# Kernel optimization log

Measured on AMD Instinct MI355X. Metric: run time of the kernel, lower is better.

## Reference

```python
import jax, jax.numpy as jnp
import numpy as np
from functools import partial

# Regular Tanner graph: (dv=3, dc=6)-regular LDPC-style code
NUM_CHKS = 512
NUM_VARS = 1024
DC = 6           # check degree
DV = 3           # variable degree
D = 16           # msg_dim
HIDDEN_MULT = 4
T = 5
BATCH = 256
E = NUM_CHKS * DC  # = NUM_VARS * DV = 3072 edges


def setup_inputs() -> dict:
    key = jax.random.key(0)
    ks = jax.random.split(key, 12)

    syndromes = jax.random.randint(ks[0], (BATCH, NUM_CHKS), 0, 2, dtype=jnp.int32)

    # Graph: edge e (check-major) belongs to check e//DC, slot e%DC.
    # perm lists edge ids in var-major order: perm[v*DV + s] = edge id.
    rng = np.random.default_rng(0)
    perm = jnp.asarray(rng.permutation(E), dtype=jnp.int32)

    prior_llr = jax.random.normal(ks[1], (NUM_VARS,), dtype=jnp.float32)

    in_c = DC * D + 1          # 97
    hid_c = HIDDEN_MULT * in_c # 388
    out_c = DC * D             # 96
    in_v = DV * D + 1          # 49
    hid_v = HIDDEN_MULT * in_v # 196
    out_v = DV * D + 1         # 49

    def lin(k, fan_in, fan_out):
        lim = 1.0 / np.sqrt(fan_in)
        kw, kb = jax.random.split(k)
        W = jax.random.uniform(kw, (fan_in, fan_out), jnp.float32, -lim, lim)
        b = jax.random.uniform(kb, (fan_out,), jnp.float32, -lim, lim)
        return W, b

    cW1, cb1 = lin(ks[2], in_c, hid_c)
    cW2, cb2 = lin(ks[3], hid_c, out_c)
    vW1, vb1 = lin(ks[4], in_v, hid_v)
    vW2, vb2 = lin(ks[5], hid_v, out_v)

    return {
        "syndromes": syndromes, "num_iters": T, "prior_llr": prior_llr,
        "perm": perm, "cW1": cW1, "cb1": cb1, "cW2": cW2, "cb2": cb2,
        "vW1": vW1, "vb1": vb1, "vW2": vW2, "vb2": vb2,
    }


def _mlp(x, W1, b1, W2, b2):
    h = jax.nn.gelu(x @ W1 + b1, approximate=False)  # torch nn.GELU default = exact
    return h @ W2 + b2


def reference(syndromes, num_iters, prior_llr, perm, cW1, cb1, cW2, cb2, vW1, vb1, vW2, vb2):
    B = syndromes.shape[0]
    sgn = (1 - 2 * syndromes).astype(jnp.float32)          # (B, C) syndrome signs
    inv_perm = jnp.argsort(perm)                            # edge -> var-major slot
    var_of_edge = inv_perm // DV                            # (E,)

    # Init var->check messages: first component = prior LLR of the edge's variable
    Mc0 = jnp.zeros((B, E, D), jnp.float32).at[:, :, 0].set(
        jnp.broadcast_to(prior_llr[var_of_edge][None, :], (B, E)))

    prior_col = jnp.broadcast_to(prior_llr[None, :, None], (B, NUM_VARS, 1))

    def step(Mc, _):
        # --- check node update (all checks have degree DC; grouped GEMM) ---
        xc = Mc.reshape(B, NUM_CHKS, DC * D)
        xc = jnp.concatenate([xc, sgn[:, :, None]], axis=-1)        # (B,C,DC*D+1)
        yc = _mlp(xc, cW1, cb1, cW2, cb2) * sgn[:, :, None]         # (B,C,DC*D)
        Mv = yc.reshape(B, E, D)                                     # check->var msgs (edge order)
        # --- variable node update (all vars have degree DV) ---
        xv = Mv[:, perm].reshape(B, NUM_VARS, DV * D)                # gather var-major
        xv = jnp.concatenate([xv, prior_col], axis=-1)               # (B,V,DV*D+1)
        yv = _mlp(xv, vW1, vb1, vW2, vb2)                            # (B,V,DV*D+1)
        llr = yv[:, :, -1]                                           # (B,V)
        Mc_new = yv[:, :, : DV * D].reshape(B, E, D)[:, inv_perm]    # scatter to edge order
        return Mc_new, llr

    _, llrs = jax.lax.scan(step, Mc0, None, length=num_iters)
    return llrs  # (T, B, NUM_VARS)
```

## Files before the change

### kernel.cpp

```cpp
#include <hip/hip_runtime.h>
#include <cstdint>
#include <cstddef>

typedef _Float16 half8 __attribute__((ext_vector_type(8)));
typedef _Float16 half4 __attribute__((ext_vector_type(4)));
typedef float floatx4 __attribute__((ext_vector_type(4)));

#define BATCH 256
#define NCHK 512
#define NVAR 1024
#define EDGE 3072

#define KC    96
#define NT1C  26
#define NT1VP 14

__device__ __forceinline__ float gelu_f(float x) {
  float ax = fabsf(x) * 0.70710678118654752440f;
  float t  = 1.0f / fmaf(0.3275911f, ax, 1.0f);
  float p  = t * (0.254829592f + t * (-0.284496736f + t * (1.421413741f +
             t * (-1.453152027f + t * 1.061405429f))));
  float e  = __expf(-ax * ax);
  float erfv = fmaf(-p, e, 1.0f);
  float s  = copysignf(erfv, x);
  float hx = 0.5f * x;
  return fmaf(hx, s, hx);
}

__device__ __forceinline__ float gelu_lut(const float2* __restrict__ tab, float x) {
  float t  = fmaf(x, 64.0f, 512.0f);
  float tc = fminf(fmaxf(t, 0.0f), 1023.0f);
  float tf = __builtin_truncf(tc);
  float fr = tc - tf;
  int idx  = (int)tf;
  float2 ns = tab[idx];
  float h  = fmaf(fr, ns.y, ns.x);
  return fmaf(fmaxf(t - tc, 0.0f), 0.015625f, h);
}

__device__ __forceinline__ void gload_lds16(const void* g, void* lds) {
  __builtin_amdgcn_global_load_lds(
      (const __attribute__((address_space(1))) unsigned int*)g,
      (__attribute__((address_space(3))) unsigned int*)lds, 16, 0, 0);
}

__global__ void pack_kernel(const float* __restrict__ cW1, const float* __restrict__ cb1,
                            const float* __restrict__ cW2, const float* __restrict__ cb2,
                            const float* __restrict__ vW1, const float* __restrict__ vb1,
                            const float* __restrict__ vW2, const float* __restrict__ vb2,
                            _Float16* __restrict__ w1c, _Float16* __restrict__ w2c,
                            _Float16* __restrict__ w1v, _Float16* __restrict__ w2v,
                            float* __restrict__ bwp, float* __restrict__ bwm,
                            float* __restrict__ b2c, float* __restrict__ b1v,
                            float* __restrict__ b2v)
{
  int id = blockIdx.x * 256 + threadIdx.x;
  const int S0 = NT1C * 3 * 64;
  const int S1 = (NT1C / 2) * 6 * 64;
  const int S2 = NT1VP * 2 * 64;
  const int S3 = (NT1VP / 2) * 4 * 64;
  if (id < S0) {
    int fh = id / 64, l = id % 64;
    int ht = fh / 3, s = fh % 3;
    int q = l >> 4, n = ht * 16 + (l & 15);
    half8 v;
    #pragma unroll
    for (int j = 0; j < 8; ++j) {
      int k = s * 32 + q * 8 + j;
      float x = (n < 388) ? cW1[k * 388 + n] : 0.0f;
      v[j] = (_Float16)x;
    }
    *(half8*)(w1c + (size_t)id * 8) = v;
    return;
  }
  id -= S0;
  if (id < S1) {
    int f = id / 64, l = id % 64;
    int htc = f / 6, nt = f % 6;
    int q = l >> 4, n = nt * 16 + (l & 15);
    int kA = 32 * htc + 4 * q;
    half8 v;
    #pragma unroll
    for (int j = 0; j < 8; ++j) {
      int k = (j < 4) ? (kA + j) : (kA + 16 + (j - 4));
      float x = (k < 388) ? cW2[k * 96 + n] : 0.0f;
      v[j] = (_Float16)x;
    }
    *(half8*)(w2c + (size_t)id * 8) = v;
    return;
  }
  id -= S1;
  if (id < S2) {
    int fh = id / 64, l = id % 64;
    int ht = fh / 2, s = fh % 2;
    int q = l >> 4, n = ht * 16 + (l & 15);
    half8 v;
    #pragma unroll
    for (int j = 0; j < 8; ++j) {
      int k = s * 32 + q * 8 + j;
      float x = (k < 49 && n < 196) ? vW1[k * 196 + n] : 0.0f;
      v[j] = (_Float16)x;
    }
    *(half8*)(w1v + (size_t)id * 8) = v;
    return;
  }
  id -= S2;
  if (id < S3) {
    int f = id / 64, l = id % 64;
    int htc = f / 4, nt = f % 4;
    int q = l >> 4, n = nt * 16 + (l & 15);
    int kA = 32 * htc + 4 * q;
    half8 v;
    #pragma unroll
    for (int j = 0; j < 8; ++j) {
      int k = (j < 4) ? (kA + j) : (kA + 16 + (j - 4));
      float x = (k < 196 && n < 49) ? vW2[k * 49 + n] : 0.0f;
      v[j] = (_Float16)x;
    }
    *(half8*)(w2v + (size_t)id * 8) = v;
    return;
  }
  id -= S3;
  if (id < 416) {
    float b = (id < 388) ? cb1[id] : 0.0f;
    float wv = (id < 388) ? cW1[96 * 388 + id] : 0.0f;
    bwp[id] = b + wv;
    return;
  }
  id -= 416;
  if (id < 416) {
    float b = (id < 388) ? cb1[id] : 0.0f;
    float wv = (id < 388) ? cW1[96 * 388 + id] : 0.0f;
    bwm[id] = b - wv;
    return;
  }
  id -= 416;
  if (id < 96)  { b2c[id]  = cb2[id]; return; }
  id -= 96;
  if (id < 224) { b1v[id]  = (id < 196) ? vb1[id] : 0.0f; return; }
  id -= 224;
  if (id < 64)  { b2v[id]  = (id < 49) ? vb2[id] : 0.0f; return; }
}

__global__ void init_kernel(const int* __restrict__ perm, const float* __restrict__ prior,
                            _Float16* __restrict__ Mc)
{
  int t = blockIdx.x * 256 + threadIdx.x;
  int b = t / EDGE, k = t - b * EDGE;
  int e = perm[k];
  _Float16* dst = Mc + ((size_t)b * EDGE + e) * 16;
  half8 z  = {0,0,0,0,0,0,0,0};
  half8 z0 = z;
  z0[0] = (_Float16)prior[k / 3];
  *(half8*)dst = z0;
  *(half8*)(dst + 8) = z;
}

#define CG1(WAOFF, HTG, H0, H1)                                                          \
  {                                                                                      \
    half8 wa0 = wb[((WAOFF) + 0) * 64 + l];                                              \
    half8 wa1 = wb[((WAOFF) + 1) * 64 + l];                                              \
    half8 wa2 = wb[((WAOFF) + 2) * 64 + l];                                              \
    floatx4 a0 = *(const floatx4*)&bwL[sel0 + (HTG) * 16 + q * 4];                       \
    floatx4 a1 = *(const floatx4*)&bwL[sel1 + (HTG) * 16 + q * 4];                       \
    a0 = __builtin_amdgcn_mfma_f32_16x16x32_f16(wa0, mb[0][0], a0, 0, 0, 0);             \
    a1 = __builtin_amdgcn_mfma_f32_16x16x32_f16(wa0, mb[1][0], a1, 0, 0, 0);             \
    a0 = __builtin_amdgcn_mfma_f32_16x16x32_f16(wa1, mb[0][1], a0, 0, 0, 0);             \
    a1 = __builtin_amdgcn_mfma_f32_16x16x32_f16(wa1, mb[1][1], a1, 0, 0, 0);             \
    a0 = __builtin_amdgcn_mfma_f32_16x16x32_f16(wa2, mb[0][2], a0, 0, 0, 0);             \
    a1 = __builtin_amdgcn_mfma_f32_16x16x32_f16(wa2, mb[1][2], a1, 0, 0, 0);             \
    _Pragma("unroll")                                                                    \
    for (int r = 0; r < 4; ++r) H0[r] = (_Float16)gelu_lut(tab, a0[r]);                  \
    _Pragma("unroll")                                                                    \
    for (int r = 0; r < 4; ++r) H1[r] = (_Float16)gelu_lut(tab, a1[r]);                  \
  }

#define CG2(H0A, H0B, H1A, H1B)                                                          \
  {                                                                                      \
    half8 hc0 = __builtin_shufflevector(H0A, H0B, 0, 1, 2, 3, 4, 5, 6, 7);               \
    half8 hc1 = __builtin_shufflevector(H1A, H1B, 0, 1, 2, 3, 4, 5, 6, 7);               \
    _Pragma("unroll")                                                                    \
    for (int nt = 0; nt < 6; ++nt) {                                                     \
      half8 wp = wb[384 + nt * 64 + l];                                                  \
      acc2[0][nt] = __builtin_amdgcn_mfma_f32_16x16x32_f16(wp, hc0, acc2[0][nt], 0,0,0); \
      acc2[1][nt] = __builtin_amdgcn_mfma_f32_16x16x32_f16(wp, hc1, acc2[1][nt], 0,0,0); \
    }                                                                                    \
  }

#define CSTAGE(CH, BUF)                                                      \
  {                                                                          \
    if (w < 2) {                                                             \
      const char* gsrc = (const char*)W1p + (size_t)(CH) * 6144;             \
      _Pragma("unroll")                                                      \
      for (int s_ = 0; s_ < 3; ++s_)                                         \
        gload_lds16(gsrc + (((w * 3 + s_) * 64 + l) << 4),                   \
                    &wbuf[BUF][(w * 3 + s_) * 64]);                          \
    } else {                                                                 \
      const char* gsrc = (const char*)W2p + (size_t)(CH) * 6144;             \
      _Pragma("unroll")                                                      \
      for (int s_ = 0; s_ < 3; ++s_)                                         \
        gload_lds16(gsrc + ((((w - 2) * 3 + s_) * 64 + l) << 4),             \
                    &wbuf[BUF][(6 + (w - 2) * 3 + s_) * 64]);                \
    }                                                                        \
  }

__global__ __launch_bounds__(256, 4) void kernelC(
    const _Float16* __restrict__ Mc, const int* __restrict__ synd,
    _Float16* __restrict__ Yc,
    const _Float16* __restrict__ W1p, const _Float16* __restrict__ W2p,
    const float* __restrict__ bwp, const float* __restrict__ bwm,
    const float* __restrict__ b2)
{
  __shared__ float2 tab[1024];
  __shared__ __attribute__((aligned(16))) float bwL[832];
  __shared__ half8 wbuf[2][768];

  const int tid = threadIdx.x, w = tid >> 6, l = tid & 63;
  const int q = l >> 4, c = l & 15;
  const int r0 = blockIdx.x * 128 + w * 32;

  CSTAGE(0, 0)

  for (int k_ = tid; k_ < 1024; k_ += 256) {
    float x_  = (k_ - 512) * 0.015625f;
    float y0_ = gelu_f(x_);
    float y1_ = gelu_f(x_ + 0.015625f);
    tab[k_] = make_float2(y0_, y1_ - y0_);
  }
  for (int k_ = tid; k_ < 416; k_ += 256) {
    bwL[k_]       = bwp[k_];
    bwL[416 + k_] = bwm[k_];
  }

  half8 mb[2][3];
  float sg[2];
  #pragma unroll
  for (int rg = 0; rg < 2; ++rg) {
    const _Float16* Arow = Mc + (size_t)(r0 + rg * 16 + c) * KC;
    #pragma unroll
    for (int ks = 0; ks < 3; ++ks)
      mb[rg][ks] = *(const half8*)(Arow + ks * 32 + q * 8);
    sg[rg] = 1.0f - 2.0f * (float)synd[r0 + rg * 16 + c];
  }
  const int sel0 = (sg[0] > 0.0f) ? 0 : 416;
  const int sel1 = (sg[1] > 0.0f) ? 0 : 416;

  floatx4 acc2[2][6];
  #pragma unroll
  for (int rg = 0; rg < 2; ++rg)
    #pragma unroll
    for (int nt = 0; nt < 6; ++nt)
      acc2[rg][nt] = (floatx4){0.f, 0.f, 0.f, 0.f};

  __syncthreads();

  int cur = 0;
  #pragma unroll 1
  for (int i = 0; i < 12; ++i) {
    CSTAGE(i + 1, cur ^ 1)
    const half8* wb = (const half8*)wbuf[cur];
    half4 h0A, h1A, h0B, h1B;
    __builtin_amdgcn_s_setprio(1);
    CG1(0, 2 * i,     h0A, h1A)
    CG1(3, 2 * i + 1, h0B, h1B)
    CG2(h0A, h0B, h1A, h1B)
    __builtin_amdgcn_s_setprio(0);
    __syncthreads();
    cur ^= 1;
  }
  {
    const half8* wb = (const half8*)wbuf[cur];
    half4 h0A, h1A;
    __builtin_amdgcn_s_setprio(1);
    CG1(0, 24, h0A, h1A)
    half4 z4 = {0, 0, 0, 0};
    CG2(h0A, z4, h1A, z4)
    __builtin_amdgcn_s_setprio(0);
  }

  #pragma unroll
  for (int rg = 0; rg < 2; ++rg) {
    const size_t row = (size_t)(r0 + rg * 16 + c);
    #pragma unroll
    for (int nt = 0; nt < 6; ++nt) {
      floatx4 bia = *(const floatx4*)(b2 + nt * 16 + q * 4);
      half4 yy;
      #pragma unroll
      for (int r = 0; r < 4; ++r)
        yy[r] = (_Float16)((acc2[rg][nt][r] + bia[r]) * sg[rg]);
      *(half4*)(Yc + row * 96 + nt * 16 + q * 4) = yy;
    }
  }
}

#define VG1(WAOFF, HTG, H0, H1)                                                          \
  {                                                                                      \
    half8 wa0 = wb[((WAOFF) + 0) * 64 + l];                                              \
    half8 wa1 = wb[((WAOFF) + 1) * 64 + l];                                              \
    floatx4 i0 = *(const floatx4*)&b1L[(HTG) * 16 + q * 4];                              \
    floatx4 a0 = i0, a1 = i0;                                                            \
    a0 = __builtin_amdgcn_mfma_f32_16x16x32_f16(wa0, mb[0][0], a0, 0, 0, 0);             \
    a1 = __builtin_amdgcn_mfma_f32_16x16x32_f16(wa0, mb[1][0], a1, 0, 0, 0);             \
    a0 = __builtin_amdgcn_mfma_f32_16x16x32_f16(wa1, mb[0][1], a0, 0, 0, 0);             \
    a1 = __builtin_amdgcn_mfma_f32_16x16x32_f16(wa1, mb[1][1], a1, 0, 0, 0);             \
    _Pragma("unroll")                                                                    \
    for (int r = 0; r < 4; ++r) H0[r] = (_Float16)gelu_lut(tab, a0[r]);                  \
    _Pragma("unroll")                                                                    \
    for (int r = 0; r < 4; ++r) H1[r] = (_Float16)gelu_lut(tab, a1[r]);                  \
  }

#define VG2(H0A, H0B, H1A, H1B)                                                          \
  {                                                                                      \
    half8 hc0 = __builtin_shufflevector(H0A, H0B, 0, 1, 2, 3, 4, 5, 6, 7);               \
    half8 hc1 = __builtin_shufflevector(H1A, H1B, 0, 1, 2, 3, 4, 5, 6, 7);               \
    _Pragma("unroll")                                                                    \
    for (int nt = 0; nt < 4; ++nt) {                                                     \
      half8 wp = wb[256 + nt * 64 + l];                                                  \
      acc2[0][nt] = __builtin_amdgcn_mfma_f32_16x16x32_f16(wp, hc0, acc2[0][nt], 0,0,0); \
      acc2[1][nt] = __builtin_amdgcn_mfma_f32_16x16x32_f16(wp, hc1, acc2[1][nt], 0,0,0); \
    }                                                                                    \
  }

#define VSTAGE(CH, BUF)                                                      \
  {                                                                          \
    if (w < 2) {                                                             \
      const char* gsrc = (const char*)W1p + (size_t)(CH) * 4096;             \
      _Pragma("unroll")                                                      \
      for (int s_ = 0; s_ < 2; ++s_)                                         \
        gload_lds16(gsrc + (((w * 2 + s_) * 64 + l) << 4),                   \
                    &wbuf[BUF][(w * 2 + s_) * 64]);                          \
    } else {                                                                 \
      const char* gsrc = (const char*)W2p + (size_t)(CH) * 4096;             \
      _Pragma("unroll")                                                      \
      for (int s_ = 0; s_ < 2; ++s_)                                         \
        gload_lds16(gsrc + ((((w - 2) * 2 + s_) * 64 + l) << 4),             \
                    &wbuf[BUF][(4 + (w - 2) * 2 + s_) * 64]);                \
    }                                                                        \
  }

__global__ __launch_bounds__(256, 4) void kernelV(
    const _Float16* __restrict__ Yc, const int* __restrict__ perm,
    const float* __restrict__ prior,
    _Float16* __restrict__ Mc, float* __restrict__ outp,
    const _Float16* __restrict__ W1p, const _Float16* __restrict__ W2p,
    const float* __restrict__ b1, const float* __restrict__ b2)
{
  __shared__ float2 tab[1024];
  __shared__ __attribute__((aligned(16))) float b1L[224];
  __shared__ half8 wbuf[2][512];

  const int tid = threadIdx.x, w = tid >> 6, l = tid & 63;
  const int q = l >> 4, c = l & 15;
  const int r0 = blockIdx.x * 128 + w * 32;
  const int b  = r0 >> 10;
  const int v0 = r0 & 1023;
  const size_t yb = (size_t)b * EDGE;

  VSTAGE(0, 0)

  for (int k_ = tid; k_ < 1024; k_ += 256) {
    float x_  = (k_ - 512) * 0.015625f;
    float y0_ = gelu_f(x_);
    float y1_ = gelu_f(x_ + 0.015625f);
    tab[k_] = make_float2(y0_, y1_ - y0_);
  }
  if (tid < 224) b1L[tid] = b1[tid];

  half8 mb[2][2];
  #pragma unroll
  for (int rg = 0; rg < 2; ++rg) {
    int v = v0 + rg * 16 + c;
    int e0 = perm[3 * v + (q >> 1)];
    mb[rg][0] = *(const half8*)(Yc + (yb + e0) * 16 + (q & 1) * 8);
    half8 m1 = {0,0,0,0,0,0,0,0};
    if (q < 2) {
      int e2 = perm[3 * v + 2];
      m1 = *(const half8*)(Yc + (yb + e2) * 16 + q * 8);
    } else if (q == 2) {
      m1[0] = (_Float16)prior[v];
    }
    mb[rg][1] = m1;
  }

  floatx4 acc2[2][4];
  #pragma unroll
  for (int rg = 0; rg < 2; ++rg)
    #pragma unroll
    for (int nt = 0; nt < 4; ++nt)
      acc2[rg][nt] = (floatx4){0.f, 0.f, 0.f, 0.f};

  __syncthreads();

  int cur = 0;
  #pragma unroll 1
  for (int i = 0; i < 6; ++i) {
    VSTAGE(i + 1, cur ^ 1)
    const half8* wb = (const half8*)wbuf[cur];
    half4 h0A, h1A, h0B, h1B;
    __builtin_amdgcn_s_setprio(1);
    VG1(0, 2 * i,     h0A, h1A)
    VG1(2, 2 * i + 1, h0B, h1B)
    VG2(h0A, h0B, h1A, h1B)
    __builtin_amdgcn_s_setprio(0);
    __syncthreads();
    cur ^= 1;
  }
  {
    const half8* wb = (const half8*)wbuf[cur];
    half4 h0A, h1A;
    __builtin_amdgcn_s_setprio(1);
    VG1(0, 12, h0A, h1A)
    half4 z4 = {0, 0, 0, 0};
    VG2(h0A, z4, h1A, z4)
    __builtin_amdgcn_s_setprio(0);
  }

  const float bllr = b2[48];
  #pragma unroll
  for (int rg = 0; rg < 2; ++rg) {
    int v = v0 + rg * 16 + c;
    #pragma unroll
    for (int nt = 0; nt < 3; ++nt) {
      int pe = perm[3 * v + nt];
      floatx4 bia = *(const floatx4*)(b2 + nt * 16 + q * 4);
      half4 yy;
      #pragma unroll
      for (int r = 0; r < 4; ++r)
        yy[r] = (_Float16)(acc2[rg][nt][r] + bia[r]);
      *(half4*)(Mc + (yb + pe) * 16 + q * 4) = yy;
    }
    if (q == 0)
      outp[r0 + rg * 16 + c] = acc2[rg][3][0] + bllr;
  }
}

extern "C" void kernel_launch(void* const* d_in, const int* in_sizes, int n_in,
                              void* d_out, int out_size, void* d_ws, size_t ws_size,
                              hipStream_t stream)
{
  const int*   synd  = (const int*)d_in[0];
  const float* prior = (const float*)d_in[2];
  const int*   perm  = (const int*)d_in[3];
  const float* cW1 = (const float*)d_in[4];
  const float* cb1 = (const float*)d_in[5];
  const float* cW2 = (const float*)d_in[6];
  const float* cb2 = (const float*)d_in[7];
  const float* vW1 = (const float*)d_in[8];
  const float* vb1 = (const float*)d_in[9];
  const float* vW2 = (const float*)d_in[10];
  const float* vb2 = (const float*)d_in[11];
  float* outp = (float*)d_out;
  const int T = out_size / (BATCH * NVAR);

  char* p = (char*)d_ws;
  _Float16* Mc  = (_Float16*)p; p += (size_t)BATCH * EDGE * 16 * 2;
  _Float16* Yc  = (_Float16*)p; p += (size_t)BATCH * EDGE * 16 * 2;
  _Float16* w1c = (_Float16*)p; p += (size_t)NT1C * 3 * 64 * 8 * 2;
  _Float16* w2c = (_Float16*)p; p += (size_t)(NT1C / 2) * 6 * 64 * 8 * 2;
  _Float16* w1v = (_Float16*)p; p += (size_t)NT1VP * 2 * 64 * 8 * 2;
  _Float16* w2v = (_Float16*)p; p += (size_t)(NT1VP / 2) * 4 * 64 * 8 * 2;
  float* bwp  = (float*)p; p += 416 * 4;
  float* bwm  = (float*)p; p += 416 * 4;
  float* b2c  = (float*)p; p += 96 * 4;
  float* b1v  = (float*)p; p += 224 * 4;
  float* b2v  = (float*)p; p += 64 * 4;

  const int packN = NT1C * 3 * 64 + (NT1C / 2) * 6 * 64 +
                    NT1VP * 2 * 64 + (NT1VP / 2) * 4 * 64 +
                    416 + 416 + 96 + 224 + 64;
  pack_kernel<<<(packN + 255) / 256, 256, 0, stream>>>(
      cW1, cb1, cW2, cb2, vW1, vb1, vW2, vb2,
      w1c, w2c, w1v, w2v, bwp, bwm, b2c, b1v, b2v);
  init_kernel<<<(BATCH * EDGE) / 256, 256, 0, stream>>>(perm, prior, Mc);

  for (int t = 0; t < T; ++t) {
    kernelC<<<(BATCH * NCHK) / 128, 256, 0, stream>>>(
        Mc, synd, Yc, w1c, w2c, bwp, bwm, b2c);
    kernelV<<<(BATCH * NVAR) / 128, 256, 0, stream>>>(
        Yc, perm, prior, Mc, outp + (size_t)t * BATCH * NVAR, w1v, w2v, b1v, b2v);
  }
}
```

Baseline: 470.5 us.

## Fuse all decoder iterations into one persistent per-batch kernel with LDS-resident messages

Replaces the init kernel and the per-iteration check and variable kernel launches with one kernel launch. Each 1024-thread block owns one batch element and keeps its whole edge-message array in shared memory for every iteration. This removes the global-memory round trips of the Mc and Yc messages and the repeated launches. In exchange, each CU runs one large block using most of its LDS, and the block does the variable update in two sequential halves with block-wide barriers between phases.

Result: slower. 549.9 us (+16.9%).

```diff
diff --git a/kernel.cpp b/kernel.cpp
--- a/kernel.cpp
+++ b/kernel.cpp
@@ -11,7 +11,6 @@
 #define NVAR 1024
 #define EDGE 3072
 
-#define KC    96
 #define NT1C  26
 #define NT1VP 14
 
@@ -142,20 +141,6 @@
   if (id < 64)  { b2v[id]  = (id < 49) ? vb2[id] : 0.0f; return; }
 }
 
-__global__ void init_kernel(const int* __restrict__ perm, const float* __restrict__ prior,
-                            _Float16* __restrict__ Mc)
-{
-  int t = blockIdx.x * 256 + threadIdx.x;
-  int b = t / EDGE, k = t - b * EDGE;
-  int e = perm[k];
-  _Float16* dst = Mc + ((size_t)b * EDGE + e) * 16;
-  half8 z  = {0,0,0,0,0,0,0,0};
-  half8 z0 = z;
-  z0[0] = (_Float16)prior[k / 3];
-  *(half8*)dst = z0;
-  *(half8*)(dst + 8) = z;
-}
-
 #define CG1(WAOFF, HTG, H0, H1)                                                          \
   {                                                                                      \
     half8 wa0 = wb[((WAOFF) + 0) * 64 + l];                                              \
@@ -189,109 +174,14 @@
 
 #define CSTAGE(CH, BUF)                                                      \
   {                                                                          \
-    if (w < 2) {                                                             \
-      const char* gsrc = (const char*)W1p + (size_t)(CH) * 6144;             \
-      _Pragma("unroll")                                                      \
-      for (int s_ = 0; s_ < 3; ++s_)                                         \
-        gload_lds16(gsrc + (((w * 3 + s_) * 64 + l) << 4),                   \
-                    &wbuf[BUF][(w * 3 + s_) * 64]);                          \
-    } else {                                                                 \
-      const char* gsrc = (const char*)W2p + (size_t)(CH) * 6144;             \
-      _Pragma("unroll")                                                      \
-      for (int s_ = 0; s_ < 3; ++s_)                                         \
-        gload_lds16(gsrc + ((((w - 2) * 3 + s_) * 64 + l) << 4),             \
-                    &wbuf[BUF][(6 + (w - 2) * 3 + s_) * 64]);                \
+    if (w < 6) {                                                             \
+      const char* gsrc = (const char*)W1c + (size_t)(CH) * 6144;             \
+      gload_lds16(gsrc + ((w * 64 + l) << 4), &wbuf[BUF][w * 64]);           \
+    } else if (w < 12) {                                                     \
+      const char* gsrc = (const char*)W2c + (size_t)(CH) * 6144;             \
+      gload_lds16(gsrc + (((w - 6) * 64 + l) << 4), &wbuf[BUF][w * 64]);     \
     }                                                                        \
   }
-
-__global__ __launch_bounds__(256, 4) void kernelC(
-    const _Float16* __restrict__ Mc, const int* __restrict__ synd,
-    _Float16* __restrict__ Yc,
-    const _Float16* __restrict__ W1p, const _Float16* __restrict__ W2p,
-    const float* __restrict__ bwp, const float* __restrict__ bwm,
-    const float* __restrict__ b2)
-{
-  __shared__ float2 tab[1024];
-  __shared__ __attribute__((aligned(16))) float bwL[832];
-  __shared__ half8 wbuf[2][768];
-
-  const int tid = threadIdx.x, w = tid >> 6, l = tid & 63;
-  const int q = l >> 4, c = l & 15;
-  const int r0 = blockIdx.x * 128 + w * 32;
-
-  CSTAGE(0, 0)
-
-  for (int k_ = tid; k_ < 1024; k_ += 256) {
-    float x_  = (k_ - 512) * 0.015625f;
-    float y0_ = gelu_f(x_);
-    float y1_ = gelu_f(x_ + 0.015625f);
-    tab[k_] = make_float2(y0_, y1_ - y0_);
-  }
-  for (int k_ = tid; k_ < 416; k_ += 256) {
-    bwL[k_]       = bwp[k_];
-    bwL[416 + k_] = bwm[k_];
-  }
-
-  half8 mb[2][3];
-  float sg[2];
-  #pragma unroll
-  for (int rg = 0; rg < 2; ++rg) {
-    const _Float16* Arow = Mc + (size_t)(r0 + rg * 16 + c) * KC;
-    #pragma unroll
-    for (int ks = 0; ks < 3; ++ks)
-      mb[rg][ks] = *(const half8*)(Arow + ks * 32 + q * 8);
-    sg[rg] = 1.0f - 2.0f * (float)synd[r0 + rg * 16 + c];
-  }
-  const int sel0 = (sg[0] > 0.0f) ? 0 : 416;
-  const int sel1 = (sg[1] > 0.0f) ? 0 : 416;
-
-  floatx4 acc2[2][6];
-  #pragma unroll
-  for (int rg = 0; rg < 2; ++rg)
-    #pragma unroll
-    for (int nt = 0; nt < 6; ++nt)
-      acc2[rg][nt] = (floatx4){0.f, 0.f, 0.f, 0.f};
-
-  __syncthreads();
-
-  int cur = 0;
-  #pragma unroll 1
-  for (int i = 0; i < 12; ++i) {
-    CSTAGE(i + 1, cur ^ 1)
-    const half8* wb = (const half8*)wbuf[cur];
-    half4 h0A, h1A, h0B, h1B;
-    __builtin_amdgcn_s_setprio(1);
-    CG1(0, 2 * i,     h0A, h1A)
-    CG1(3, 2 * i + 1, h0B, h1B)
-    CG2(h0A, h0B, h1A, h1B)
-    __builtin_amdgcn_s_setprio(0);
-    __syncthreads();
-    cur ^= 1;
-  }
-  {
-    const half8* wb = (const half8*)wbuf[cur];
-    half4 h0A, h1A;
-    __builtin_amdgcn_s_setprio(1);
-    CG1(0, 24, h0A, h1A)
-    half4 z4 = {0, 0, 0, 0};
-    CG2(h0A, z4, h1A, z4)
-    __builtin_amdgcn_s_setprio(0);
-  }
-
-  #pragma unroll
-  for (int rg = 0; rg < 2; ++rg) {
-    const size_t row = (size_t)(r0 + rg * 16 + c);
-    #pragma unroll
-    for (int nt = 0; nt < 6; ++nt) {
-      floatx4 bia = *(const floatx4*)(b2 + nt * 16 + q * 4);
-      half4 yy;
-      #pragma unroll
-      for (int r = 0; r < 4; ++r)
-        yy[r] = (_Float16)((acc2[rg][nt][r] + bia[r]) * sg[rg]);
-      *(half4*)(Yc + row * 96 + nt * 16 + q * 4) = yy;
-    }
-  }
-}
 
 #define VG1(WAOFF, HTG, H0, H1)                                                          \
   {                                                                                      \
@@ -323,114 +213,202 @@
 
 #define VSTAGE(CH, BUF)                                                      \
   {                                                                          \
-    if (w < 2) {                                                             \
-      const char* gsrc = (const char*)W1p + (size_t)(CH) * 4096;             \
-      _Pragma("unroll")                                                      \
-      for (int s_ = 0; s_ < 2; ++s_)                                         \
-        gload_lds16(gsrc + (((w * 2 + s_) * 64 + l) << 4),                   \
-                    &wbuf[BUF][(w * 2 + s_) * 64]);                          \
-    } else {                                                                 \
-      const char* gsrc = (const char*)W2p + (size_t)(CH) * 4096;             \
-      _Pragma("unroll")                                                      \
-      for (int s_ = 0; s_ < 2; ++s_)                                         \
-        gload_lds16(gsrc + ((((w - 2) * 2 + s_) * 64 + l) << 4),             \
-                    &wbuf[BUF][(4 + (w - 2) * 2 + s_) * 64]);                \
+    if (w < 4) {                                                             \
+      const char* gsrc = (const char*)W1v + (size_t)(CH) * 4096;             \
+      gload_lds16(gsrc + ((w * 64 + l) << 4), &wbuf[BUF][w * 64]);           \
+    } else if (w < 8) {                                                      \
+      const char* gsrc = (const char*)W2v + (size_t)(CH) * 4096;             \
+      gload_lds16(gsrc + (((w - 4) * 64 + l) << 4), &wbuf[BUF][w * 64]);     \
     }                                                                        \
   }
 
-__global__ __launch_bounds__(256, 4) void kernelV(
-    const _Float16* __restrict__ Yc, const int* __restrict__ perm,
-    const float* __restrict__ prior,
-    _Float16* __restrict__ Mc, float* __restrict__ outp,
-    const _Float16* __restrict__ W1p, const _Float16* __restrict__ W2p,
-    const float* __restrict__ b1, const float* __restrict__ b2)
+__global__ __launch_bounds__(1024, 1) void fused(
+    const int* __restrict__ synd, const int* __restrict__ perm,
+    const float* __restrict__ prior, float* __restrict__ outp,
+    const _Float16* __restrict__ W1c, const _Float16* __restrict__ W2c,
+    const _Float16* __restrict__ W1v, const _Float16* __restrict__ W2v,
+    const float* __restrict__ bwp, const float* __restrict__ bwm,
+    const float* __restrict__ b2c, const float* __restrict__ b1vv,
+    const float* __restrict__ b2v, int T)
 {
+  __shared__ _Float16 mcyc[EDGE * 16];
+  __shared__ half8 wbuf[2][768];
   __shared__ float2 tab[1024];
+  __shared__ __attribute__((aligned(16))) float bwL[832];
   __shared__ __attribute__((aligned(16))) float b1L[224];
-  __shared__ half8 wbuf[2][512];
-
+
+  const int b = blockIdx.x;
   const int tid = threadIdx.x, w = tid >> 6, l = tid & 63;
   const int q = l >> 4, c = l & 15;
-  const int r0 = blockIdx.x * 128 + w * 32;
-  const int b  = r0 >> 10;
-  const int v0 = r0 & 1023;
-  const size_t yb = (size_t)b * EDGE;
-
-  VSTAGE(0, 0)
-
-  for (int k_ = tid; k_ < 1024; k_ += 256) {
+
+  for (int k_ = tid; k_ < 1024; k_ += 1024) {
     float x_  = (k_ - 512) * 0.015625f;
     float y0_ = gelu_f(x_);
     float y1_ = gelu_f(x_ + 0.015625f);
     tab[k_] = make_float2(y0_, y1_ - y0_);
   }
-  if (tid < 224) b1L[tid] = b1[tid];
-
-  half8 mb[2][2];
+  if (tid < 416) { bwL[tid] = bwp[tid]; bwL[416 + tid] = bwm[tid]; }
+  if (tid < 224) b1L[tid] = b1vv[tid];
+
   #pragma unroll
-  for (int rg = 0; rg < 2; ++rg) {
-    int v = v0 + rg * 16 + c;
-    int e0 = perm[3 * v + (q >> 1)];
-    mb[rg][0] = *(const half8*)(Yc + (yb + e0) * 16 + (q & 1) * 8);
-    half8 m1 = {0,0,0,0,0,0,0,0};
-    if (q < 2) {
-      int e2 = perm[3 * v + 2];
-      m1 = *(const half8*)(Yc + (yb + e2) * 16 + q * 8);
-    } else if (q == 2) {
-      m1[0] = (_Float16)prior[v];
-    }
-    mb[rg][1] = m1;
-  }
-
-  floatx4 acc2[2][4];
-  #pragma unroll
-  for (int rg = 0; rg < 2; ++rg)
-    #pragma unroll
-    for (int nt = 0; nt < 4; ++nt)
-      acc2[rg][nt] = (floatx4){0.f, 0.f, 0.f, 0.f};
+  for (int kk = 0; kk < 3; ++kk) {
+    int k = kk * 1024 + tid;
+    int e = perm[k];
+    half8 z = {0, 0, 0, 0, 0, 0, 0, 0};
+    half8 z0 = z;
+    z0[0] = (_Float16)prior[k / 3];
+    *(half8*)(mcyc + e * 16) = z0;
+    *(half8*)(mcyc + e * 16 + 8) = z;
+  }
+
+  const int rL = w * 32;
+  const float sgv0 = 1.0f - 2.0f * (float)synd[b * 512 + rL + c];
+  const float sgv1 = 1.0f - 2.0f * (float)synd[b * 512 + rL + 16 + c];
+  const int sel0 = (sgv0 > 0.0f) ? 0 : 416;
+  const int sel1 = (sgv1 > 0.0f) ? 0 : 416;
 
   __syncthreads();
 
-  int cur = 0;
   #pragma unroll 1
-  for (int i = 0; i < 6; ++i) {
-    VSTAGE(i + 1, cur ^ 1)
-    const half8* wb = (const half8*)wbuf[cur];
-    half4 h0A, h1A, h0B, h1B;
-    __builtin_amdgcn_s_setprio(1);
-    VG1(0, 2 * i,     h0A, h1A)
-    VG1(2, 2 * i + 1, h0B, h1B)
-    VG2(h0A, h0B, h1A, h1B)
-    __builtin_amdgcn_s_setprio(0);
+  for (int t = 0; t < T; ++t) {
+    {
+      CSTAGE(0, 0)
+
+      half8 mb[2][3];
+      #pragma unroll
+      for (int rg = 0; rg < 2; ++rg) {
+        const _Float16* mrow = mcyc + (size_t)(rL + rg * 16 + c) * 96;
+        #pragma unroll
+        for (int ks = 0; ks < 3; ++ks)
+          mb[rg][ks] = *(const half8*)(mrow + ks * 32 + q * 8);
+      }
+
+      floatx4 acc2[2][6];
+      #pragma unroll
+      for (int rg = 0; rg < 2; ++rg)
+        #pragma unroll
+        for (int nt = 0; nt < 6; ++nt)
+          acc2[rg][nt] = (floatx4){0.f, 0.f, 0.f, 0.f};
+
+      __syncthreads();
+
+      int cur = 0;
+      #pragma unroll 1
+      for (int i = 0; i < 12; ++i) {
+        CSTAGE(i + 1, cur ^ 1)
+        const half8* wb = (const half8*)wbuf[cur];
+        half4 h0A, h1A, h0B, h1B;
+        __builtin_amdgcn_s_setprio(1);
+        CG1(0, 2 * i,     h0A, h1A)
+        CG1(3, 2 * i + 1, h0B, h1B)
+        CG2(h0A, h0B, h1A, h1B)
+        __builtin_amdgcn_s_setprio(0);
+        __syncthreads();
+        cur ^= 1;
+      }
+      {
+        const half8* wb = (const half8*)wbuf[cur];
+        half4 h0A, h1A;
+        __builtin_amdgcn_s_setprio(1);
+        CG1(0, 24, h0A, h1A)
+        half4 z4 = {0, 0, 0, 0};
+        CG2(h0A, z4, h1A, z4)
+        __builtin_amdgcn_s_setprio(0);
+      }
+
+      #pragma unroll
+      for (int rg = 0; rg < 2; ++rg) {
+        _Float16* yrow = mcyc + (size_t)(rL + rg * 16 + c) * 96;
+        const float sg = rg ? sgv1 : sgv0;
+        #pragma unroll
+        for (int nt = 0; nt < 6; ++nt) {
+          floatx4 bia = *(const floatx4*)(b2c + nt * 16 + q * 4);
+          half4 yy;
+          #pragma unroll
+          for (int r = 0; r < 4; ++r)
+            yy[r] = (_Float16)((acc2[rg][nt][r] + bia[r]) * sg);
+          *(half4*)(yrow + nt * 16 + q * 4) = yy;
+        }
+      }
+    }
+
     __syncthreads();
-    cur ^= 1;
-  }
-  {
-    const half8* wb = (const half8*)wbuf[cur];
-    half4 h0A, h1A;
-    __builtin_amdgcn_s_setprio(1);
-    VG1(0, 12, h0A, h1A)
-    half4 z4 = {0, 0, 0, 0};
-    VG2(h0A, z4, h1A, z4)
-    __builtin_amdgcn_s_setprio(0);
-  }
-
-  const float bllr = b2[48];
-  #pragma unroll
-  for (int rg = 0; rg < 2; ++rg) {
-    int v = v0 + rg * 16 + c;
-    #pragma unroll
-    for (int nt = 0; nt < 3; ++nt) {
-      int pe = perm[3 * v + nt];
-      floatx4 bia = *(const floatx4*)(b2 + nt * 16 + q * 4);
-      half4 yy;
-      #pragma unroll
-      for (int r = 0; r < 4; ++r)
-        yy[r] = (_Float16)(acc2[rg][nt][r] + bia[r]);
-      *(half4*)(Mc + (yb + pe) * 16 + q * 4) = yy;
-    }
-    if (q == 0)
-      outp[r0 + rg * 16 + c] = acc2[rg][3][0] + bllr;
+
+    float* op = outp + (size_t)t * (BATCH * NVAR) + (size_t)b * NVAR;
+    #pragma unroll 1
+    for (int p = 0; p < 2; ++p) {
+      VSTAGE(0, 0)
+
+      const int vbase = p * 512 + w * 32;
+      half8 mb[2][2];
+      #pragma unroll
+      for (int rg = 0; rg < 2; ++rg) {
+        int v = vbase + rg * 16 + c;
+        int e0 = perm[3 * v + (q >> 1)];
+        mb[rg][0] = *(const half8*)(mcyc + e0 * 16 + (q & 1) * 8);
+        half8 m1 = {0, 0, 0, 0, 0, 0, 0, 0};
+        if (q < 2) {
+          int e2 = perm[3 * v + 2];
+          m1 = *(const half8*)(mcyc + e2 * 16 + q * 8);
+        } else if (q == 2) {
+          m1[0] = (_Float16)prior[v];
+        }
+        mb[rg][1] = m1;
+      }
+
+      floatx4 acc2[2][4];
+      #pragma unroll
+      for (int rg = 0; rg < 2; ++rg)
+        #pragma unroll
+        for (int nt = 0; nt < 4; ++nt)
+          acc2[rg][nt] = (floatx4){0.f, 0.f, 0.f, 0.f};
+
+      __syncthreads();
+
+      int cur = 0;
+      #pragma unroll 1
+      for (int i = 0; i < 6; ++i) {
+        VSTAGE(i + 1, cur ^ 1)
+        const half8* wb = (const half8*)wbuf[cur];
+        half4 h0A, h1A, h0B, h1B;
+        __builtin_amdgcn_s_setprio(1);
+        VG1(0, 2 * i,     h0A, h1A)
+        VG1(2, 2 * i + 1, h0B, h1B)
+        VG2(h0A, h0B, h1A, h1B)
+        __builtin_amdgcn_s_setprio(0);
+        __syncthreads();
+        cur ^= 1;
+      }
+      {
+        const half8* wb = (const half8*)wbuf[cur];
+        half4 h0A, h1A;
+        __builtin_amdgcn_s_setprio(1);
+        VG1(0, 12, h0A, h1A)
+        half4 z4 = {0, 0, 0, 0};
+        VG2(h0A, z4, h1A, z4)
+        __builtin_amdgcn_s_setprio(0);
+      }
+
+      const float bllr = b2v[48];
+      #pragma unroll
+      for (int rg = 0; rg < 2; ++rg) {
+        int v = vbase + rg * 16 + c;
+        #pragma unroll
+        for (int nt = 0; nt < 3; ++nt) {
+          int pe = perm[3 * v + nt];
+          floatx4 bia = *(const floatx4*)(b2v + nt * 16 + q * 4);
+          half4 yy;
+          #pragma unroll
+          for (int r = 0; r < 4; ++r)
+            yy[r] = (_Float16)(acc2[rg][nt][r] + bia[r]);
+          *(half4*)(mcyc + pe * 16 + q * 4) = yy;
+        }
+        if (q == 0)
+          op[v] = acc2[rg][3][0] + bllr;
+      }
+
+      __syncthreads();
+    }
   }
 }
 
@@ -450,11 +428,9 @@
   const float* vW2 = (const float*)d_in[10];
   const float* vb2 = (const float*)d_in[11];
   float* outp = (float*)d_out;
-  const int T = out_size / (BATCH * NVAR);
+  int T = out_size / (BATCH * NVAR);
 
   char* p = (char*)d_ws;
-  _Float16* Mc  = (_Float16*)p; p += (size_t)BATCH * EDGE * 16 * 2;
-  _Float16* Yc  = (_Float16*)p; p += (size_t)BATCH * EDGE * 16 * 2;
   _Float16* w1c = (_Float16*)p; p += (size_t)NT1C * 3 * 64 * 8 * 2;
   _Float16* w2c = (_Float16*)p; p += (size_t)(NT1C / 2) * 6 * 64 * 8 * 2;
   _Float16* w1v = (_Float16*)p; p += (size_t)NT1VP * 2 * 64 * 8 * 2;
@@ -471,12 +447,8 @@
   pack_kernel<<<(packN + 255) / 256, 256, 0, stream>>>(
       cW1, cb1, cW2, cb2, vW1, vb1, vW2, vb2,
       w1c, w2c, w1v, w2v, bwp, bwm, b2c, b1v, b2v);
-  init_kernel<<<(BATCH * EDGE) / 256, 256, 0, stream>>>(perm, prior, Mc);
-
-  for (int t = 0; t < T; ++t) {
-    kernelC<<<(BATCH * NCHK) / 128, 256, 0, stream>>>(
-        Mc, synd, Yc, w1c, w2c, bwp, bwm, b2c);
-    kernelV<<<(BATCH * NVAR) / 128, 256, 0, stream>>>(
-        Yc, perm, prior, Mc, outp + (size_t)t * BATCH * NVAR, w1v, w2v, b1v, b2v);
-  }
-}
+
+  fused<<<BATCH, 1024, 0, stream>>>(
+      synd, perm, prior, outp, w1c, w2c, w1v, w2v,
+      bwp, bwm, b2c, b1v, b2v, T);
+}
```
